# Kernel optimization log

Hardware: AMD Instinct MI355X
Metric: run time of the kernel (lower is better)

Reference implementation:

```python
import jax, jax.numpy as jnp
import numpy as np

WEIGHT = 1.0  # config['weight']


def setup_inputs() -> dict:
    key = jax.random.key(0)
    ks = jax.random.split(key, 10)
    B, N, S, C, D, E, H, V = 8, 4096, 512, 16, 1024, 256, 1024, 100000
    return {
        "span_vecs": jax.random.normal(ks[0], (B, N, D), jnp.float32),
        "ent_table": jax.random.normal(ks[1], (V, E), jnp.float32) * 0.02,
        "W1": jax.random.normal(ks[2], (D + E, H), jnp.float32) * (1.0 / np.sqrt(D + E)),
        "b1": jnp.zeros((H,), jnp.float32),
        "W2": jax.random.normal(ks[3], (H,), jnp.float32) * (1.0 / np.sqrt(H)),
        "b2": jnp.zeros((), jnp.float32),
        "targets_all": jax.random.uniform(ks[4], (B, N, C), jnp.float32),
        "linker_indices": jax.random.randint(ks[5], (B, S), 0, N, jnp.int32),
        "candidates_all": jax.random.randint(ks[6], (B, N, C), 0, V, jnp.int32),
        "candidate_lengths_all": jax.random.randint(ks[7], (B, N), 0, C + 1, jnp.int32),
    }


def reference(span_vecs, ent_table, W1, b1, W2, b2, targets_all,
              linker_indices, candidates_all, candidate_lengths_all):
    D = span_vecs.shape[-1]
    C = candidates_all.shape[-1]
    idx = linker_indices  # [B, S]

    # batched_index_select gathers over the span axis
    candidates = jnp.take_along_axis(candidates_all, idx[:, :, None], axis=1)        # [B,S,C] int
    lengths = jnp.take_along_axis(candidate_lengths_all, idx, axis=1)                # [B,S] int
    targets = jnp.take_along_axis(targets_all, idx[:, :, None], axis=1)              # [B,S,C]
    linker_vecs = jnp.take_along_axis(span_vecs, idx[:, :, None], axis=1)            # [B,S,D]

    cand_vecs = ent_table[candidates]                                                # [B,S,C,E]

    # layers: Linear(D+E,H) -> ReLU -> (dropout=identity in eval) -> Linear(H,1)
    # fused: split W1 so the [B,S,C,D+E] expanded concat is never materialized
    W1s, W1e = W1[:D], W1[D:]
    h_span = jnp.einsum('bsd,dh->bsh', linker_vecs, W1s)                             # [B,S,H]
    h_cand = jnp.einsum('bsce,eh->bsch', cand_vecs, W1e)                             # [B,S,C,H]
    h = jax.nn.relu(h_span[:, :, None, :] + h_cand + b1)
    scores = jnp.einsum('bsch,h->bsc', h, W2) + b2                                   # [B,S,C]

    # create_candidate_mask
    mask = (jnp.arange(C)[None, None, :] < lengths[:, :, None]).astype(scores.dtype)

    # BCEWithLogitsLoss(reduction='none'), masked sum * weight
    bce = jnp.maximum(scores, 0.0) - scores * targets + jnp.log1p(jnp.exp(-jnp.abs(scores)))
    loss = (mask * bce).sum() * WEIGHT

    predictions = jnp.argmax(scores - (1.0 - mask) * 1e23, axis=-1)                  # [B,S]
    return loss, scores, predictions
```

## Files before the change

### kernel.cpp

```cpp
#include <hip/hip_runtime.h>
#include <math.h>


typedef short short8 __attribute__((ext_vector_type(8)));
typedef _Float16 half8v __attribute__((ext_vector_type(8)));
typedef float f32x16 __attribute__((ext_vector_type(16)));

static __device__ inline unsigned short f2bf(float x) {
  unsigned u = __float_as_uint(x);
  unsigned r = (u + 0x7FFFu + ((u >> 16) & 1u)) >> 16;
  return (unsigned short)r;
}
static __device__ inline float bf2f(unsigned short b) {
  return __uint_as_float(((unsigned)b) << 16);
}
static __device__ inline unsigned short f2h(float x) {
  _Float16 h = (_Float16)x;
  return *(unsigned short*)&h;
}

#define GLD_TO_LDS(gp, lp)                                          \
  __builtin_amdgcn_global_load_lds(                                 \
      (const __attribute__((address_space(1))) void*)(gp),          \
      (__attribute__((address_space(3))) void*)(lp), 16, 0, 0)

static __device__ inline void split_write(unsigned short* buf, int g,
                                          float4 c0, float4 c1) {
  float xs[8] = {c0.x, c0.y, c0.z, c0.w, c1.x, c1.y, c1.z, c1.w};
  short8 h8, l8;
#pragma unroll
  for (int j = 0; j < 8; ++j) {
    unsigned short h = f2bf(xs[j]);
    h8[j] = (short)h;
    l8[j] = (short)f2bf(xs[j] - bf2f(h));
  }
  *(short8*)(buf + (g << 3)) = h8;
  *(short8*)(buf + 4096 + (g << 3)) = l8;
}

__global__ __launch_bounds__(256) void k_prep_e(
    const float* __restrict__ ent, const float* __restrict__ W1,
    const int* __restrict__ linker, const int* __restrict__ cand_all,
    unsigned short* __restrict__ A2, unsigned short* __restrict__ sThi,
    unsigned short* __restrict__ sTlo, unsigned short* __restrict__ eT16) {
  __shared__ float t[32][33];
  const int bx = blockIdx.x;
  if (bx < 16384) {
    int f = bx * 256 + threadIdx.x;
    int row = f >> 6;
    int pair = row >> 4;
    int b = pair >> 9;
    int i = linker[pair];
    int cid = cand_all[(((size_t)b << 12) + (size_t)i) * 16 + (row & 15)];
    const float4 v = *((const float4*)(ent + ((size_t)cid << 8)) + (f & 63));
    *(ushort4*)(A2 + ((size_t)f << 2)) =
        make_ushort4(f2h(v.x), f2h(v.y), f2h(v.z), f2h(v.w));
  } else {
    int b2x = bx - 16384;
    int n0 = (b2x & 31) * 32, k0 = (b2x >> 5) * 32;
    int rr = threadIdx.x >> 5, cc = threadIdx.x & 31;
#pragma unroll
    for (int i = 0; i < 4; ++i)
      t[rr + 8 * i][cc] = W1[(size_t)(k0 + rr + 8 * i) * 1024 + n0 + cc];
    __syncthreads();
#pragma unroll
    for (int i = 0; i < 4; ++i) {
      int nl = rr + 8 * i;
      float v = t[cc][nl];
      int n = n0 + nl, k = k0 + cc;
      if (k0 < 1024) {
        unsigned short h = f2bf(v);
        unsigned short l = f2bf(v - bf2f(h));
        sThi[(size_t)n * 1024 + k] = h;
        sTlo[(size_t)n * 1024 + k] = l;
      } else {
        eT16[(size_t)n * 256 + (k - 1024)] = f2h(v);
      }
    }
  }
}

template <int KSTEPS>
__global__ __launch_bounds__(256, 2) void k_g32g(
    const float* __restrict__ span, const int* __restrict__ linker,
    const unsigned short* __restrict__ Bhi, const unsigned short* __restrict__ Blo,
    float* __restrict__ Out) {
  const int tid = threadIdx.x;
  const int l = tid & 63;
  const int w = tid >> 6;
  const int wm = w >> 1, wn = w & 1;
  const int id = blockIdx.x;
  const int z = id >> 8;
  const int sid = id & 255;
  const int m8 = sid & 7;
  const int cb = (sid >> 3) & 7;
  const int q = sid >> 6;
  const int row0 = ((q << 3) + m8) << 7;
  const int col0 = cb << 7;
  const int koff = z * (KSTEPS * 32);
  Out += (size_t)z * 4194304;

  __shared__ unsigned short lds[32768];

  f32x16 acc[2][2];
#pragma unroll
  for (int i = 0; i < 2; ++i)
#pragma unroll
    for (int j = 0; j < 2; ++j)
#pragma unroll
      for (int k = 0; k < 16; ++k) acc[i][j][k] = 0.f;

  const int ar0 = tid >> 2, ap0 = tid & 3;
  const int al0c = ap0 ^ ((ar0 >> 1) & 3);
  const int ar1 = ar0 + 64;
  const int al1c = ap0 ^ ((ar1 >> 1) & 3);
  const int r0g = row0 + ar0, r1g = row0 + ar1;
  const float* asrc0 =
      span + (((size_t)(r0g >> 9) << 12) + linker[r0g]) * 1024 + koff + al0c * 8;
  const float* asrc1 =
      span + (((size_t)(r1g >> 9) << 12) + linker[r1g]) * 1024 + koff + al1c * 8;
  const size_t boff0 = (size_t)(col0 + ar0) * 1024 + al0c * 8 + koff;
  const size_t boff1 = (size_t)(col0 + ar1) * 1024 + al1c * 8 + koff;
  const int w512 = w * 512;

  {
    float4 a00 = *(const float4*)(asrc0);
    float4 a01 = *(const float4*)(asrc0 + 4);
    float4 a10 = *(const float4*)(asrc1);
    float4 a11 = *(const float4*)(asrc1 + 4);
    GLD_TO_LDS(Bhi + boff0, lds + 8192 + w512);
    GLD_TO_LDS(Bhi + boff1, lds + 10240 + w512);
    GLD_TO_LDS(Blo + boff0, lds + 12288 + w512);
    GLD_TO_LDS(Blo + boff1, lds + 14336 + w512);
    split_write(lds, tid, a00, a01);
    split_write(lds, tid + 256, a10, a11);
  }
  asm volatile("s_waitcnt vmcnt(0) lgkmcnt(0)" ::: "memory");
  __builtin_amdgcn_s_barrier();
  asm volatile("" ::: "memory");

  for (int ks = 0; ks < KSTEPS; ++ks) {
    float4 a00, a01, a10, a11;
    const int k0n = (ks + 1) * 32;
    unsigned short* bn = lds + (((ks + 1) & 1) << 14);
    if (ks + 1 < KSTEPS) {
      a00 = *(const float4*)(asrc0 + k0n);
      a01 = *(const float4*)(asrc0 + k0n + 4);
      a10 = *(const float4*)(asrc1 + k0n);
      a11 = *(const float4*)(asrc1 + k0n + 4);
      GLD_TO_LDS(Bhi + boff0 + k0n, bn + 8192 + w512);
      GLD_TO_LDS(Bhi + boff1 + k0n, bn + 10240 + w512);
      GLD_TO_LDS(Blo + boff0 + k0n, bn + 12288 + w512);
      GLD_TO_LDS(Blo + boff1 + k0n, bn + 14336 + w512);
    }

    const unsigned short* cbuf = lds + ((ks & 1) << 14);
#pragma unroll
    for (int kc = 0; kc < 2; ++kc) {
      const int kg = kc * 2 + (l >> 5);
      short8 ah[2], alv[2], bh[2], bl[2];
#pragma unroll
      for (int it = 0; it < 2; ++it) {
        int r = wm * 64 + it * 32 + (l & 31);
        int off = r * 32 + ((kg ^ ((r >> 1) & 3)) << 3);
        ah[it] = *(const short8*)(cbuf + off);
        alv[it] = *(const short8*)(cbuf + 4096 + off);
      }
#pragma unroll
      for (int jt = 0; jt < 2; ++jt) {
        int r = wn * 64 + jt * 32 + (l & 31);
        int off = r * 32 + ((kg ^ ((r >> 1) & 3)) << 3);
        bh[jt] = *(const short8*)(cbuf + 8192 + off);
        bl[jt] = *(const short8*)(cbuf + 12288 + off);
      }
#pragma unroll
      for (int it = 0; it < 2; ++it)
#pragma unroll
        for (int jt = 0; jt < 2; ++jt) {
          acc[it][jt] = __builtin_amdgcn_mfma_f32_32x32x16_bf16(
              ah[it], bh[jt], acc[it][jt], 0, 0, 0);
          acc[it][jt] = __builtin_amdgcn_mfma_f32_32x32x16_bf16(
              ah[it], bl[jt], acc[it][jt], 0, 0, 0);
          acc[it][jt] = __builtin_amdgcn_mfma_f32_32x32x16_bf16(
              alv[it], bh[jt], acc[it][jt], 0, 0, 0);
        }
    }

    if (ks + 1 < KSTEPS) {
      split_write(bn, tid, a00, a01);
      split_write(bn, tid + 256, a10, a11);
      asm volatile("s_waitcnt vmcnt(0) lgkmcnt(0)" ::: "memory");
      __builtin_amdgcn_s_barrier();
      asm volatile("" ::: "memory");
    }
  }

#pragma unroll
  for (int it = 0; it < 2; ++it) {
    int mb = row0 + wm * 64 + it * 32 + 4 * (l >> 5);
#pragma unroll
    for (int jt = 0; jt < 2; ++jt) {
      int n = col0 + wn * 64 + jt * 32 + (l & 31);
#pragma unroll
      for (int rg = 0; rg < 16; ++rg) {
        int m = mb + (rg & 3) + 8 * (rg >> 2);
        Out[(size_t)m * 1024 + n] = acc[it][jt][rg];
      }
    }
  }
}

__global__ __launch_bounds__(256, 2) void k_gf16(
    const unsigned short* __restrict__ A,
    const unsigned short* __restrict__ Bt,
    const float* __restrict__ HsIn, const float* __restrict__ b1,
    const float* __restrict__ W2, float* __restrict__ Out) {
  const int tid = threadIdx.x;
  const int l = tid & 63;
  const int w = tid >> 6;
  const int id = blockIdx.x;
  const int m8 = id & 7;
  const int cb = (id >> 3) & 7;
  const int q = id >> 6;
  const int row0 = ((q << 3) + m8) << 8;
  const int col0 = cb << 7;

  __shared__ unsigned short lds[36864];

  f32x16 acc[2][4];
#pragma unroll
  for (int i = 0; i < 2; ++i)
#pragma unroll
    for (int j = 0; j < 4; ++j)
#pragma unroll
      for (int k = 0; k < 16; ++k) acc[i][j][k] = 0.f;

  const int ar = tid >> 2, ap = tid & 3;
  const int ac = ap ^ ((ar >> 1) & 3);
  const size_t abase = (size_t)(row0 + ar) * 256 + ac * 8;
  const size_t bbase = (size_t)(col0 + ar) * 256 + ac * 8;
  const int w512 = w * 512;

#define STAGE2(buf, ks32)                                         \
  do {                                                            \
    GLD_TO_LDS(A + abase + (ks32), (buf) + w512);                 \
    GLD_TO_LDS(A + abase + 16384 + (ks32), (buf) + 2048 + w512);  \
    GLD_TO_LDS(A + abase + 32768 + (ks32), (buf) + 4096 + w512);  \
    GLD_TO_LDS(A + abase + 49152 + (ks32), (buf) + 6144 + w512);  \
    GLD_TO_LDS(Bt + bbase + (ks32), (buf) + 8192 + w512);         \
    GLD_TO_LDS(Bt + bbase + 16384 + (ks32), (buf) + 10240 + w512);\
  } while (0)

  STAGE2(lds, 0);
  STAGE2(lds + 12288, 32);
  asm volatile("s_waitcnt vmcnt(6)" ::: "memory");
  __builtin_amdgcn_s_barrier();
  asm volatile("" ::: "memory");

#pragma unroll
  for (int ks = 0; ks < 8; ++ks) {
    if (ks + 2 < 8) {
      unsigned short* bn = lds + ((ks + 2) % 3) * 12288;
      STAGE2(bn, (ks + 2) * 32);
    }

    const unsigned short* cbuf = lds + (ks % 3) * 12288;
#pragma unroll
    for (int kc = 0; kc < 2; ++kc) {
      const int kg = kc * 2 + (l >> 5);
      half8v av[2], bv[4];
#pragma unroll
      for (int it = 0; it < 2; ++it) {
        int r = w * 64 + it * 32 + (l & 31);
        int off = r * 32 + ((kg ^ ((r >> 1) & 3)) << 3);
        av[it] = *(const half8v*)(cbuf + off);
      }
#pragma unroll
      for (int jt = 0; jt < 4; ++jt) {
        int r = jt * 32 + (l & 31);
        int off = 8192 + r * 32 + ((kg ^ ((r >> 1) & 3)) << 3);
        bv[jt] = *(const half8v*)(cbuf + off);
      }
      __builtin_amdgcn_s_setprio(1);
#pragma unroll
      for (int it = 0; it < 2; ++it)
#pragma unroll
        for (int jt = 0; jt < 4; ++jt)
          acc[it][jt] = __builtin_amdgcn_mfma_f32_32x32x16_f16(
              av[it], bv[jt], acc[it][jt], 0, 0, 0);
      __builtin_amdgcn_s_setprio(0);
    }

    if (ks + 1 < 8) {
      if (ks + 2 < 8) {
        asm volatile("s_waitcnt vmcnt(6)" ::: "memory");
      } else {
        asm volatile("s_waitcnt vmcnt(0)" ::: "memory");
      }
      __builtin_amdgcn_s_barrier();
      asm volatile("" ::: "memory");
    }
  }
#undef STAGE2

  float sv[2][16];
#pragma unroll
  for (int it = 0; it < 2; ++it) {
#pragma unroll
    for (int rg = 0; rg < 16; ++rg) sv[it][rg] = 0.f;
    const int p0 = (row0 + w * 64 + it * 32) >> 4;
#pragma unroll
    for (int jt = 0; jt < 4; ++jt) {
      int n = col0 + jt * 32 + (l & 31);
      float b1v = b1[n], w2v = W2[n];
      float add0 = HsIn[(size_t)p0 * 1024 + n] +
                   HsIn[4194304 + (size_t)p0 * 1024 + n] + b1v;
      float add1 = HsIn[(size_t)(p0 + 1) * 1024 + n] +
                   HsIn[4194304 + (size_t)(p0 + 1) * 1024 + n] + b1v;
#pragma unroll
      for (int rg = 0; rg < 16; ++rg) {
        float h = fmaxf(acc[it][jt][rg] + (rg < 8 ? add0 : add1), 0.f);
        sv[it][rg] = fmaf(h, w2v, sv[it][rg]);
      }
    }
  }
  __syncthreads();
  float* scf = (float*)lds;
  const int cc0 = l & 31, lh4 = 4 * (l >> 5);
#pragma unroll
  for (int it = 0; it < 2; ++it)
#pragma unroll
    for (int rg = 0; rg < 16; ++rg) {
      int row = (rg & 3) + 8 * (rg >> 2) + lh4;
      scf[((w * 2 + it) * 32 + row) * 32 + ((cc0 + row) & 31)] = sv[it][rg];
    }
  __syncthreads();
  int gr = tid;
  int wv = gr >> 6, itv = (gr >> 5) & 1, r = gr & 31;
  const float* srow = scf + ((wv * 2 + itv) * 32 + r) * 32;
  float sum = 0.f;
#pragma unroll
  for (int j = 0; j < 32; ++j) sum += srow[(j + r) & 31];
  Out[(size_t)cb * 65536 + row0 + gr] = sum;
}

__global__ __launch_bounds__(64) void k_final8(const float* __restrict__ score8,
                                               const float* __restrict__ b2p,
                                               const float* __restrict__ targets_all,
                                               const int* __restrict__ linker,
                                               const int* __restrict__ len_all,
                                               float* __restrict__ out) {
  int p = blockIdx.x * 64 + threadIdx.x;
  float b2 = b2p[0];
  int b = p >> 9;
  int i = linker[p];
  int len = len_all[(b << 12) + i];
  const float* tg = targets_all + ((((size_t)b << 12) + (size_t)i) << 4);

  float sc[16];
#pragma unroll
  for (int c = 0; c < 16; ++c) sc[c] = b2;
#pragma unroll
  for (int c8 = 0; c8 < 8; ++c8) {
    const float4* q4 = (const float4*)(score8 + (size_t)c8 * 65536 + p * 16);
#pragma unroll
    for (int j = 0; j < 4; ++j) {
      float4 v = q4[j];
      sc[j * 4 + 0] += v.x; sc[j * 4 + 1] += v.y;
      sc[j * 4 + 2] += v.z; sc[j * 4 + 3] += v.w;
    }
  }

  float loss = 0.f;
  float best = -INFINITY;
  int bc = 0;
#pragma unroll
  for (int c = 0; c < 16; ++c) {
    float s = sc[c];
    out[1 + p * 16 + c] = s;
    float val;
    if (c < len) {
      float t = tg[c];
      loss += fmaxf(s, 0.f) - s * t + log1pf(expf(-fabsf(s)));
      val = s;
    } else {
      val = s - 1e23f;
    }
    if (val > best) { best = val; bc = c; }
  }
  out[1 + 65536 + p] = (float)bc;

  for (int off = 32; off > 0; off >>= 1) loss += __shfl_down(loss, off, 64);
  if (threadIdx.x == 0) atomicAdd(out, loss);
}

#define BM 128
#define BN 128
#define BK 16
#define PAD 4

__global__ __launch_bounds__(256) void k_prep(const int* __restrict__ linker,
                                              const int* __restrict__ cand_all,
                                              int* __restrict__ cand_ids) {
  int g = blockIdx.x * 256 + threadIdx.x;
  int pair = g >> 4;
  int c = g & 15;
  int b = pair >> 9;
  int i = linker[pair];
  cand_ids[g] = cand_all[(((size_t)b << 12) + (size_t)i) * 16 + c];
}

__global__ __launch_bounds__(256) void k_hs(const float* __restrict__ span,
                                            const float* __restrict__ W1,
                                            const int* __restrict__ linker,
                                            float* __restrict__ Hs) {
  const int tid = threadIdx.x;
  const int tx = tid & 15, ty = tid >> 4;
  const int row0 = blockIdx.y * BM;
  const int col0 = blockIdx.x * BN;
  __shared__ float As[BK][BM + PAD];
  __shared__ float Bs[BK][BN + PAD];
  __shared__ int rows_g[BM];
  if (tid < BM) {
    int m = row0 + tid;
    int b = m >> 9;
    rows_g[tid] = (b << 12) + linker[m];
  }
  __syncthreads();
  float acc[8][8] = {};
  for (int k0 = 0; k0 < 1024; k0 += BK) {
#pragma unroll
    for (int ll = 0; ll < 2; ++ll) {
      int f = tid + ll * 256;
      int r = f >> 2;
      int kk = (f & 3) << 2;
      const float4 v = *(const float4*)(span + (size_t)rows_g[r] * 1024 + k0 + kk);
      As[kk + 0][r] = v.x; As[kk + 1][r] = v.y;
      As[kk + 2][r] = v.z; As[kk + 3][r] = v.w;
    }
#pragma unroll
    for (int ll = 0; ll < 2; ++ll) {
      int f = tid + ll * 256;
      int kk = f >> 5;
      int nn = (f & 31) << 2;
      *(float4*)&Bs[kk][nn] = *(const float4*)(W1 + (size_t)(k0 + kk) * 1024 + col0 + nn);
    }
    __syncthreads();
#pragma unroll
    for (int k = 0; k < BK; ++k) {
      float a[8], b[8];
      *(float4*)&a[0] = *(const float4*)&As[k][ty * 8];
      *(float4*)&a[4] = *(const float4*)&As[k][ty * 8 + 4];
      *(float4*)&b[0] = *(const float4*)&Bs[k][tx * 8];
      *(float4*)&b[4] = *(const float4*)&Bs[k][tx * 8 + 4];
#pragma unroll
      for (int i = 0; i < 8; ++i)
#pragma unroll
        for (int j = 0; j < 8; ++j) acc[i][j] = fmaf(a[i], b[j], acc[i][j]);
    }
    __syncthreads();
  }
#pragma unroll
  for (int i = 0; i < 8; ++i) {
    int m = row0 + ty * 8 + i;
    float* dst = Hs + (size_t)m * 1024 + col0 + tx * 8;
    *(float4*)dst = *(float4*)&acc[i][0];
    *(float4*)(dst + 4) = *(float4*)&acc[i][4];
  }
}

__global__ __launch_bounds__(256) void k_hc(const float* __restrict__ ent,
                                            const float* __restrict__ W1,
                                            const int* __restrict__ cand_ids,
                                            const float* __restrict__ Hs,
                                            const float* __restrict__ b1,
                                            const float* __restrict__ W2,
                                            float* __restrict__ score_ws) {
  const int tid = threadIdx.x;
  const int tx = tid & 15, ty = tid >> 4;
  const int row0 = blockIdx.y * BM;
  const int col0 = blockIdx.x * BN;
  __shared__ float As[BK][BM + PAD];
  __shared__ float Bs[BK][BN + PAD];
  __shared__ int rows_g[BM];
  __shared__ float red[BM][17];
  if (tid < BM) rows_g[tid] = cand_ids[row0 + tid];
  __syncthreads();
  float acc[8][8] = {};
  for (int k0 = 0; k0 < 256; k0 += BK) {
#pragma unroll
    for (int ll = 0; ll < 2; ++ll) {
      int f = tid + ll * 256;
      int r = f >> 2;
      int kk = (f & 3) << 2;
      const float4 v = *(const float4*)(ent + (size_t)rows_g[r] * 256 + k0 + kk);
      As[kk + 0][r] = v.x; As[kk + 1][r] = v.y;
      As[kk + 2][r] = v.z; As[kk + 3][r] = v.w;
    }
#pragma unroll
    for (int ll = 0; ll < 2; ++ll) {
      int f = tid + ll * 256;
      int kk = f >> 5;
      int nn = (f & 31) << 2;
      *(float4*)&Bs[kk][nn] =
          *(const float4*)(W1 + (size_t)(1024 + k0 + kk) * 1024 + col0 + nn);
    }
    __syncthreads();
#pragma unroll
    for (int k = 0; k < BK; ++k) {
      float a[8], b[8];
      *(float4*)&a[0] = *(const float4*)&As[k][ty * 8];
      *(float4*)&a[4] = *(const float4*)&As[k][ty * 8 + 4];
      *(float4*)&b[0] = *(const float4*)&Bs[k][tx * 8];
      *(float4*)&b[4] = *(const float4*)&Bs[k][tx * 8 + 4];
#pragma unroll
      for (int i = 0; i < 8; ++i)
#pragma unroll
        for (int j = 0; j < 8; ++j) acc[i][j] = fmaf(a[i], b[j], acc[i][j]);
    }
    __syncthreads();
  }
  const int pair = (row0 + ty * 8) >> 4;
  float hsv[8], b1v[8], w2v[8];
  {
    const float* hp = Hs + (size_t)pair * 1024 + col0 + tx * 8;
    *(float4*)&hsv[0] = *(const float4*)hp;
    *(float4*)&hsv[4] = *(const float4*)(hp + 4);
    const float* bp = b1 + col0 + tx * 8;
    *(float4*)&b1v[0] = *(const float4*)bp;
    *(float4*)&b1v[4] = *(const float4*)(bp + 4);
    const float* wp = W2 + col0 + tx * 8;
    *(float4*)&w2v[0] = *(const float4*)wp;
    *(float4*)&w2v[4] = *(const float4*)(wp + 4);
  }
#pragma unroll
  for (int i = 0; i < 8; ++i) {
    float s = 0.f;
#pragma unroll
    for (int j = 0; j < 8; ++j) {
      float h = acc[i][j] + hsv[j] + b1v[j];
      h = fmaxf(h, 0.f);
      s = fmaf(h, w2v[j], s);
    }
    red[ty * 8 + i][tx] = s;
  }
  __syncthreads();
  if (tid < BM) {
    float s = 0.f;
#pragma unroll
    for (int x = 0; x < 16; ++x) s += red[tid][x];
    atomicAdd(&score_ws[row0 + tid], s);
  }
}

__global__ __launch_bounds__(256) void k_final(const float* __restrict__ score_ws,
                                               const float* __restrict__ b2p,
                                               const float* __restrict__ targets_all,
                                               const int* __restrict__ linker,
                                               const int* __restrict__ len_all,
                                               float* __restrict__ out) {
  int p = blockIdx.x * 256 + threadIdx.x;
  float b2 = b2p[0];
  int b = p >> 9;
  int i = linker[p];
  int len = len_all[(b << 12) + i];
  const float* tg = targets_all + ((((size_t)b << 12) + (size_t)i) << 4);

  float loss = 0.f;
  float best = -INFINITY;
  int bc = 0;
#pragma unroll
  for (int c = 0; c < 16; ++c) {
    float sc = score_ws[p * 16 + c] + b2;
    out[1 + p * 16 + c] = sc;
    float val;
    if (c < len) {
      float t = tg[c];
      loss += fmaxf(sc, 0.f) - sc * t + log1pf(expf(-fabsf(sc)));
      val = sc;
    } else {
      val = sc - 1e23f;
    }
    if (val > best) { best = val; bc = c; }
  }
  out[1 + 65536 + p] = (float)bc;

  for (int off = 32; off > 0; off >>= 1) loss += __shfl_down(loss, off, 64);
  if ((threadIdx.x & 63) == 0) atomicAdd(out, loss);
}

extern "C" void kernel_launch(void* const* d_in, const int* in_sizes, int n_in,
                              void* d_out, int out_size, void* d_ws,
                              size_t ws_size, hipStream_t stream) {
  const float* span    = (const float*)d_in[0];
  const float* ent     = (const float*)d_in[1];
  const float* W1      = (const float*)d_in[2];
  const float* b1      = (const float*)d_in[3];
  const float* W2      = (const float*)d_in[4];
  const float* b2      = (const float*)d_in[5];
  const float* targets = (const float*)d_in[6];
  const int* linker    = (const int*)d_in[7];
  const int* cand_all  = (const int*)d_in[8];
  const int* len_all   = (const int*)d_in[9];
  float* out = (float*)d_out;

  char* ws = (char*)d_ws;
  float* Hs       = (float*)(ws + 0);
  float* score8   = (float*)(ws + 33554432);
  unsigned short* A2   = (unsigned short*)(ws + 35651584);
  unsigned short* sTh  = (unsigned short*)(ws + 69206016);
  unsigned short* sTl  = (unsigned short*)(ws + 71303168);
  unsigned short* eT16 = (unsigned short*)(ws + 73400320);
  float* score_ws = (float*)(ws + 73924608);
  int* cand_ids   = (int*)(ws + 74186752);
  const size_t NEED_MFMA = 74448896;

  hipMemsetAsync(d_out, 0, sizeof(float), stream);

  if (ws_size >= NEED_MFMA) {
    k_prep_e<<<dim3(17664), dim3(256), 0, stream>>>(
        ent, W1, linker, cand_all, A2, sTh, sTl, eT16);
    k_g32g<16><<<dim3(512), dim3(256), 0, stream>>>(span, linker, sTh, sTl, Hs);
    k_gf16<<<dim3(2048), dim3(256), 0, stream>>>(A2, eT16, Hs, b1, W2, score8);
    k_final8<<<dim3(64), dim3(64), 0, stream>>>(score8, b2, targets, linker,
                                                len_all, out);
  } else {
    hipMemsetAsync(score_ws, 0, 65536 * sizeof(float), stream);
    k_prep<<<dim3(256), dim3(256), 0, stream>>>(linker, cand_all, cand_ids);
    dim3 g1(8, 32);
    k_hs<<<g1, dim3(256), 0, stream>>>(span, W1, linker, Hs);
    dim3 g2(8, 512);
    k_hc<<<g2, dim3(256), 0, stream>>>(ent, W1, cand_ids, Hs, b1, W2, score_ws);
    k_final<<<dim3(16), dim3(256), 0, stream>>>(score_ws, b2, targets, linker,
                                                len_all, out);
  }
}
```

Before: 328.5 us.

## Triple-buffer B tiles with two-step lookahead and raise MFMA wave priority

```diff
diff --git a/kernel.cpp b/kernel.cpp
--- a/kernel.cpp
+++ b/kernel.cpp
@@ -100,7 +100,7 @@
   const int koff = z * (KSTEPS * 32);
   Out += (size_t)z * 4194304;
 
-  __shared__ unsigned short lds[32768];
+  __shared__ unsigned short lds[40960];
 
   f32x16 acc[2][2];
 #pragma unroll
@@ -123,38 +123,44 @@
   const size_t boff1 = (size_t)(col0 + ar1) * 1024 + al1c * 8 + koff;
   const int w512 = w * 512;
 
+#define STAGE_B(q3, k032)                                                \
+  do {                                                                   \
+    unsigned short* bb = lds + 16384 + (q3) * 8192;                      \
+    GLD_TO_LDS(Bhi + boff0 + (k032), bb + w512);                         \
+    GLD_TO_LDS(Bhi + boff1 + (k032), bb + 2048 + w512);                  \
+    GLD_TO_LDS(Blo + boff0 + (k032), bb + 4096 + w512);                  \
+    GLD_TO_LDS(Blo + boff1 + (k032), bb + 6144 + w512);                  \
+  } while (0)
+
   {
     float4 a00 = *(const float4*)(asrc0);
     float4 a01 = *(const float4*)(asrc0 + 4);
     float4 a10 = *(const float4*)(asrc1);
     float4 a11 = *(const float4*)(asrc1 + 4);
-    GLD_TO_LDS(Bhi + boff0, lds + 8192 + w512);
-    GLD_TO_LDS(Bhi + boff1, lds + 10240 + w512);
-    GLD_TO_LDS(Blo + boff0, lds + 12288 + w512);
-    GLD_TO_LDS(Blo + boff1, lds + 14336 + w512);
+    asm volatile("" ::: "memory");
+    STAGE_B(0, 0);
+    if (1 < KSTEPS) STAGE_B(1, 32);
     split_write(lds, tid, a00, a01);
     split_write(lds, tid + 256, a10, a11);
   }
-  asm volatile("s_waitcnt vmcnt(0) lgkmcnt(0)" ::: "memory");
+  asm volatile("s_waitcnt vmcnt(4) lgkmcnt(0)" ::: "memory");
   __builtin_amdgcn_s_barrier();
   asm volatile("" ::: "memory");
 
   for (int ks = 0; ks < KSTEPS; ++ks) {
     float4 a00, a01, a10, a11;
-    const int k0n = (ks + 1) * 32;
-    unsigned short* bn = lds + (((ks + 1) & 1) << 14);
     if (ks + 1 < KSTEPS) {
+      const int k0n = (ks + 1) * 32;
       a00 = *(const float4*)(asrc0 + k0n);
       a01 = *(const float4*)(asrc0 + k0n + 4);
       a10 = *(const float4*)(asrc1 + k0n);
       a11 = *(const float4*)(asrc1 + k0n + 4);
-      GLD_TO_LDS(Bhi + boff0 + k0n, bn + 8192 + w512);
-      GLD_TO_LDS(Bhi + boff1 + k0n, bn + 10240 + w512);
-      GLD_TO_LDS(Blo + boff0 + k0n, bn + 12288 + w512);
-      GLD_TO_LDS(Blo + boff1 + k0n, bn + 14336 + w512);
-    }
-
-    const unsigned short* cbuf = lds + ((ks & 1) << 14);
+    }
+    asm volatile("" ::: "memory");
+    if (ks + 2 < KSTEPS) STAGE_B((ks + 2) % 3, (ks + 2) * 32);
+
+    const unsigned short* cbufA = lds + (ks & 1) * 8192;
+    const unsigned short* cbufB = lds + 16384 + (ks % 3) * 8192;
 #pragma unroll
     for (int kc = 0; kc < 2; ++kc) {
       const int kg = kc * 2 + (l >> 5);
@@ -163,16 +169,17 @@
       for (int it = 0; it < 2; ++it) {
         int r = wm * 64 + it * 32 + (l & 31);
         int off = r * 32 + ((kg ^ ((r >> 1) & 3)) << 3);
-        ah[it] = *(const short8*)(cbuf + off);
-        alv[it] = *(const short8*)(cbuf + 4096 + off);
+        ah[it] = *(const short8*)(cbufA + off);
+        alv[it] = *(const short8*)(cbufA + 4096 + off);
       }
 #pragma unroll
       for (int jt = 0; jt < 2; ++jt) {
         int r = wn * 64 + jt * 32 + (l & 31);
         int off = r * 32 + ((kg ^ ((r >> 1) & 3)) << 3);
-        bh[jt] = *(const short8*)(cbuf + 8192 + off);
-        bl[jt] = *(const short8*)(cbuf + 12288 + off);
-      }
+        bh[jt] = *(const short8*)(cbufB + off);
+        bl[jt] = *(const short8*)(cbufB + 4096 + off);
+      }
+      __builtin_amdgcn_s_setprio(1);
 #pragma unroll
       for (int it = 0; it < 2; ++it)
 #pragma unroll
@@ -184,16 +191,23 @@
           acc[it][jt] = __builtin_amdgcn_mfma_f32_32x32x16_bf16(
               alv[it], bh[jt], acc[it][jt], 0, 0, 0);
         }
+      __builtin_amdgcn_s_setprio(0);
     }
 
     if (ks + 1 < KSTEPS) {
-      split_write(bn, tid, a00, a01);
-      split_write(bn, tid + 256, a10, a11);
-      asm volatile("s_waitcnt vmcnt(0) lgkmcnt(0)" ::: "memory");
+      unsigned short* bnA = lds + ((ks + 1) & 1) * 8192;
+      split_write(bnA, tid, a00, a01);
+      split_write(bnA, tid + 256, a10, a11);
+      if (ks + 2 < KSTEPS) {
+        asm volatile("s_waitcnt vmcnt(4) lgkmcnt(0)" ::: "memory");
+      } else {
+        asm volatile("s_waitcnt vmcnt(0) lgkmcnt(0)" ::: "memory");
+      }
       __builtin_amdgcn_s_barrier();
       asm volatile("" ::: "memory");
     }
   }
+#undef STAGE_B
 
 #pragma unroll
   for (int it = 0; it < 2; ++it) {
```

Result: no change. 328.8 us (+0.1%).
